# Optimization experiments

Measured on AMD Instinct MI355X. Metric: run time of the kernel, lower is better.

## Reference

```python
import jax, jax.numpy as jnp
import numpy as np
import math

B, S, D, H = 1, 2048, 2048, 16
HD = D // H  # head_dim = 128


def _rotate_half(x):
    h = x.shape[-1] // 2
    return jnp.concatenate([-x[..., h:], x[..., :h]], axis=-1)


def setup_inputs() -> dict:
    key = jax.random.key(0)
    ks = jax.random.split(key, 8)
    hidden_states = jax.random.normal(ks[0], (B, S, D), dtype=jnp.float32)
    # additive causal mask: 0 on/below diagonal, large negative above
    causal = jnp.tril(jnp.ones((S, S), dtype=bool))
    attention_mask = jnp.where(causal, 0.0, -1e9).astype(jnp.float32)[None, None]
    # LLaMA rotary tables for head_dim
    inv_freq = 1.0 / (10000.0 ** (jnp.arange(0, HD, 2, dtype=jnp.float32) / HD))
    t = jnp.arange(S, dtype=jnp.float32)
    freqs = jnp.einsum('s,d->sd', t, inv_freq)          # [S, HD/2]
    emb = jnp.concatenate([freqs, freqs], axis=-1)       # [S, HD]
    cos = jnp.cos(emb)[None, None]                       # [1,1,S,HD]
    sin = jnp.sin(emb)[None, None]
    scale = 1.0 / math.sqrt(D)
    Wq = jax.random.normal(ks[1], (D, D), dtype=jnp.float32) * scale
    Wk = jax.random.normal(ks[2], (D, D), dtype=jnp.float32) * scale
    Wv = jax.random.normal(ks[3], (D, D), dtype=jnp.float32) * scale
    Wo = jax.random.normal(ks[4], (D, D), dtype=jnp.float32) * scale
    # IA3 scales initialized to ones (as in module), perturbed slightly to be non-trivial
    l_k = jnp.ones((1, H, 1, HD), dtype=jnp.float32) + 0.01 * jax.random.normal(ks[5], (1, H, 1, HD), dtype=jnp.float32)
    l_v = jnp.ones((1, H, 1, HD), dtype=jnp.float32) + 0.01 * jax.random.normal(ks[6], (1, H, 1, HD), dtype=jnp.float32)
    return {
        'hidden_states': hidden_states, 'attention_mask': attention_mask,
        'cos': cos, 'sin': sin,
        'Wq': Wq, 'Wk': Wk, 'Wv': Wv, 'Wo': Wo, 'l_k': l_k, 'l_v': l_v,
    }


def reference(hidden_states, attention_mask, cos, sin, Wq, Wk, Wv, Wo, l_k, l_v):
    b, s, d = hidden_states.shape
    h, hd = H, HD
    # projections (nn.Linear: x @ W.T), split heads -> [b, h, s, hd]
    def split_heads(x):
        return x.reshape(b, s, h, hd).transpose(0, 2, 1, 3)
    q = split_heads(hidden_states @ Wq.T)
    k = split_heads(hidden_states @ Wk.T)
    v = split_heads(hidden_states @ Wv.T)
    # RoPE on q and k
    q = q * cos + _rotate_half(q) * sin
    k = k * cos + _rotate_half(k) * sin
    # IA3: note the module scales QUERY by peft_l_k and VALUE by peft_l_v
    q = q * l_k
    v = v * l_v
    # manual attention
    scores = jnp.einsum('bhqd,bhkd->bhqk', q, k) / math.sqrt(hd)
    scores = scores + attention_mask
    attn = jax.nn.softmax(scores.astype(jnp.float32), axis=-1).astype(scores.dtype)
    out = jnp.einsum('bhqk,bhkd->bhqd', attn, v)
    out = out.transpose(0, 2, 1, 3).reshape(b, s, d)
    return out @ Wo.T
```

## Files before the change

kernel.cpp:

```cpp
#include <hip/hip_runtime.h>

typedef __attribute__((ext_vector_type(8))) short short8;
typedef __attribute__((ext_vector_type(4))) short s16x4;
typedef __attribute__((ext_vector_type(4))) float f32x4;
typedef unsigned short ushort;

#define S_LEN 2048
#define D_MODEL 2048
#define NH 16
#define HD 128

__device__ __forceinline__ float b2f(ushort u) {
  union { unsigned int i; float f; } v; v.i = ((unsigned int)u) << 16; return v.f;
}
__device__ __forceinline__ ushort f2b(float f) {
  union { float f; unsigned int i; } v; v.f = f;
  unsigned int r = v.i + 0x7FFFu + ((v.i >> 16) & 1u);
  return (ushort)(r >> 16);
}
__device__ __forceinline__ ushort f2b_trunc(float f) {
  union { float f; unsigned int i; } v; v.f = f;
  return (ushort)(v.i >> 16);
}

__device__ __forceinline__ void gload_lds16(const void* g, void* l) {
  __builtin_amdgcn_global_load_lds(
      (const __attribute__((address_space(1))) void*)g,
      (__attribute__((address_space(3))) void*)l, 16, 0, 0);
}

template<bool C32, bool QKVM>
__device__ __forceinline__ void gemm_bf16_body(const ushort* __restrict__ A,
                                               const ushort* __restrict__ B,
                                               void* __restrict__ Cp, int ldc,
                                               const float* __restrict__ lv,
                                               const float* __restrict__ cosb,
                                               const float* __restrict__ sinb,
                                               const float* __restrict__ lk)
{
  __shared__ ushort lA[128 * 64];
  __shared__ ushort lB[128 * 64];
  const int tid  = threadIdx.x;
  const int lane = tid & 63;
  const int wave = tid >> 6;
  const int quad = lane >> 4;
  const int l15  = lane & 15;
  const int wm   = wave >> 1;
  const int wn   = wave & 1;
  const int m0   = blockIdx.y * 128;
  const int n0   = blockIdx.x * 128;

  const bool isV = QKVM && (n0 >= 4096);
  int bcol[4];
#pragma unroll
  for (int j = 0; j < 4; ++j)
    bcol[j] = (QKVM && !isV) ? (wn * 32 + (j & 1) * 16 + (j >> 1) * 64)
                             : (wn * 64 + j * 16);

  f32x4 acc[4][4];
#pragma unroll
  for (int i = 0; i < 4; ++i)
#pragma unroll
    for (int j = 0; j < 4; ++j)
      acc[i][j] = (f32x4){0.f, 0.f, 0.f, 0.f};

  const int srow0 = wave * 8 + (lane >> 3);
  const int cph   = lane & 7;

  for (int kt = 0; kt < 32; ++kt) {
    __syncthreads();
#pragma unroll
    for (int j = 0; j < 4; ++j) {
      const int row = j * 32 + srow0;
      const int gc  = cph ^ (row & 7);
      gload_lds16(A + (size_t)(m0 + row) * 2048 + kt * 64 + gc * 8,
                  &lA[row * 64 + cph * 8]);
      gload_lds16(B + (size_t)(n0 + row) * 2048 + kt * 64 + gc * 8,
                  &lB[row * 64 + cph * 8]);
    }
    __syncthreads();
#pragma unroll
    for (int kk = 0; kk < 2; ++kk) {
      short8 af[4], bfr[4];
#pragma unroll
      for (int i = 0; i < 4; ++i) {
        const int r = wm * 64 + i * 16 + l15;
        af[i] = *(const short8*)&lA[r * 64 + (((kk * 4 + quad) ^ (l15 & 7)) * 8)];
      }
#pragma unroll
      for (int j = 0; j < 4; ++j) {
        const int r = bcol[j] + l15;
        bfr[j] = *(const short8*)&lB[r * 64 + (((kk * 4 + quad) ^ (l15 & 7)) * 8)];
      }
#pragma unroll
      for (int i = 0; i < 4; ++i)
#pragma unroll
        for (int j = 0; j < 4; ++j)
          acc[i][j] = __builtin_amdgcn_mfma_f32_16x16x32_bf16(af[i], bfr[j], acc[i][j], 0, 0, 0);
    }
  }

  if (QKVM) {
    ushort* C = (ushort*)Cp;
    if (isV) {
#pragma unroll
      for (int j = 0; j < 4; ++j)
#pragma unroll
        for (int i = 0; i < 4; ++i) {
          const int vcol = n0 - 4096 + bcol[j] + l15;
          const float sc = lv[vcol];
          const int sb   = m0 + wm * 64 + i * 16 + quad * 4;
          s16x4 pk;
#pragma unroll
          for (int r = 0; r < 4; ++r) pk[r] = (short)f2b(acc[i][j][r] * sc);
          *(s16x4*)&C[(size_t)vcol * 6144 + 4096 + sb] = pk;
        }
    } else {
      const bool isQ = (n0 < 2048);
      const int hb = n0 & 2047;
      const float qsc = 0.08838834764831845f * 1.4426950408889634f;
#pragma unroll
      for (int i = 0; i < 4; ++i)
#pragma unroll
        for (int j = 0; j < 2; ++j) {
          const int d_lo = bcol[j] + l15;
          const int d_hi = d_lo + 64;
          const float sl_lo = isQ ? lk[hb + d_lo] * qsc : 1.f;
          const float sl_hi = isQ ? lk[hb + d_hi] * qsc : 1.f;
#pragma unroll
          for (int r = 0; r < 4; ++r) {
            const int s = m0 + wm * 64 + i * 16 + quad * 4 + r;
            const float c_lo = cosb[s * HD + d_lo], s_lo = sinb[s * HD + d_lo];
            const float c_hi = cosb[s * HD + d_hi], s_hi = sinb[s * HD + d_hi];
            const float lo = acc[i][j][r];
            const float hi = acc[i][j + 2][r];
            float o_lo = lo * c_lo - hi * s_lo;
            float o_hi = hi * c_hi + lo * s_hi;
            if (isQ) { o_lo *= sl_lo; o_hi *= sl_hi; }
            C[(size_t)s * 6144 + n0 + d_lo] = f2b(o_lo);
            C[(size_t)s * 6144 + n0 + d_hi] = f2b(o_hi);
          }
        }
    }
    return;
  }

#pragma unroll
  for (int i = 0; i < 4; ++i)
#pragma unroll
    for (int j = 0; j < 4; ++j)
#pragma unroll
      for (int r = 0; r < 4; ++r) {
        const int row = m0 + wm * 64 + i * 16 + quad * 4 + r;
        const int col = n0 + bcol[j] + l15;
        if (C32) ((float*)Cp)[(size_t)row * ldc + col] = acc[i][j][r];
        else     ((ushort*)Cp)[(size_t)row * ldc + col] = f2b(acc[i][j][r]);
      }
}

__global__ __launch_bounds__(256)
void gemm_qkv_b(const ushort* __restrict__ A, const ushort* __restrict__ B,
                ushort* __restrict__ C, const float* __restrict__ lv,
                const float* __restrict__ cosb, const float* __restrict__ sinb,
                const float* __restrict__ lk)
{ gemm_bf16_body<false, true>(A, B, C, 6144, lv, cosb, sinb, lk); }

__global__ __launch_bounds__(256)
void gemm_bf16_f(const ushort* __restrict__ A, const ushort* __restrict__ B,
                 float* __restrict__ C, int ldc)
{ gemm_bf16_body<true, false>(A, B, C, ldc, nullptr, nullptr, nullptr, nullptr); }

__global__ __launch_bounds__(256)
void cvt_to_bf16(const float* __restrict__ hs, const float* __restrict__ Wq,
                 const float* __restrict__ Wk, const float* __restrict__ Wv,
                 const float* __restrict__ Wo, ushort* __restrict__ dst)
{
  const size_t base = ((size_t)blockIdx.x * 256 + threadIdx.x) * 8;
  const int row = (int)(base >> 11);
  const int col = (int)(base & 2047);
  const float* src;
  if      (row < 2048) src = Wq + (size_t)row * 2048;
  else if (row < 4096) src = Wk + (size_t)(row - 2048) * 2048;
  else if (row < 6144) src = Wv + (size_t)(row - 4096) * 2048;
  else if (row < 8192) src = Wo + (size_t)(row - 6144) * 2048;
  else                 src = hs + (size_t)(row - 8192) * 2048;
  float4 a = *(const float4*)(src + col);
  float4 b = *(const float4*)(src + col + 4);
  short8 s;
  s[0] = (short)f2b(a.x); s[1] = (short)f2b(a.y);
  s[2] = (short)f2b(a.z); s[3] = (short)f2b(a.w);
  s[4] = (short)f2b(b.x); s[5] = (short)f2b(b.y);
  s[6] = (short)f2b(b.z); s[7] = (short)f2b(b.w);
  *(short8*)(dst + base) = s;
}

__device__ const int FA_QT[30]   = {5,11,11,10,10,15,15,4,9,9,13,14,14,14,15,8,8,12,12,13,13,3,7,7,12,6,6,2,1,0};
__device__ const int FA_BEG[30]  = {0,0,12,0,11,10,21,0,0,10,18,0,10,20,0,0,9,8,17,0,9,0,0,8,0,0,7,0,0,0};
__device__ const int FA_END[30]  = {12,12,24,11,22,21,32,10,10,20,28,10,20,30,10,9,18,17,26,9,18,8,8,16,8,7,14,6,4,2};
__device__ const int FA_SLOT[30] = {5,16,17,14,15,28,29,4,12,13,23,24,25,26,27,10,11,19,20,21,22,3,8,9,18,6,7,2,1,0};
__device__ const int FA_OFF[16]  = {0,1,2,3,4,5,6,8,10,12,14,16,18,21,24,27};
__device__ const int FA_NC[16]   = {1,1,1,1,1,1,2,2,2,2,2,2,3,3,3,3};

__global__ __launch_bounds__(256, 2)
void flash_attn2(const ushort* __restrict__ arena,
                 ushort* __restrict__ Ab,
                 ushort* __restrict__ Opart,
                 float* __restrict__ Ml)
{
  __shared__ ushort Kl[64 * 128];
  __shared__ ushort Vt[128 * 64];
  __shared__ ushort Pl[4][32 * 72];

  const int tid  = threadIdx.x;
  const int lane = tid & 63;
  const int w    = tid >> 6;
  const int quad = lane >> 4;
  const int l15  = lane & 15;
  const int h    = blockIdx.y;

  const int item  = blockIdx.x;
  const int qt    = FA_QT[item];
  const int ktBeg = FA_BEG[item];
  const int ktEnd = FA_END[item];
  const int slot  = h * 30 + FA_SLOT[item];

  short8 qa[2][4];
#pragma unroll
  for (int i = 0; i < 2; ++i)
#pragma unroll
    for (int kk = 0; kk < 4; ++kk)
      qa[i][kk] = *(const short8*)(arena +
          (size_t)(qt * 128 + w * 32 + i * 16 + l15) * 6144 + h * HD + kk * 32 + quad * 8);

  f32x4 o[2][8], acc_l[2];
#pragma unroll
  for (int i = 0; i < 2; ++i) {
    acc_l[i] = (f32x4){0.f, 0.f, 0.f, 0.f};
#pragma unroll
    for (int nf = 0; nf < 8; ++nf) o[i][nf] = (f32x4){0.f, 0.f, 0.f, 0.f};
  }

  short8 bones;
#pragma unroll
  for (int e = 0; e < 8; ++e) bones[e] = (short)0x3F80;

  const int ksrow0 = w * 4 + (lane >> 4);
  const int kch    = lane & 15;
  const int vrow0  = w * 8 + (lane >> 3);
  const int vch    = lane & 7;

  for (int kt = ktBeg; kt < ktEnd; ++kt) {
    __syncthreads();

#pragma unroll
    for (int j = 0; j < 4; ++j) {
      const int row = j * 16 + ksrow0;
      const int gc  = kch ^ (row & 15);
      gload_lds16(arena + (size_t)(kt * 64 + row) * 6144 + 2048 + h * HD + gc * 8,
                  &Kl[row * 128 + kch * 8]);
    }
#pragma unroll
    for (int j = 0; j < 4; ++j) {
      const int d  = j * 32 + vrow0;
      const int gc = vch ^ (d & 7);
      gload_lds16(arena + (size_t)(h * HD + d) * 6144 + 4096 + kt * 64 + gc * 8,
                  &Vt[d * 64 + vch * 8]);
    }
    __syncthreads();

    f32x4 sf[2][4];
#pragma unroll
    for (int i = 0; i < 2; ++i)
#pragma unroll
      for (int n = 0; n < 4; ++n) sf[i][n] = (f32x4){0.f, 0.f, 0.f, 0.f};
#pragma unroll
    for (int kk = 0; kk < 4; ++kk)
#pragma unroll
      for (int n = 0; n < 4; ++n) {
        const int key = n * 16 + l15;
        short8 b = *(const short8*)&Kl[key * 128 + (((kk * 4 + quad) ^ l15) * 8)];
#pragma unroll
        for (int i = 0; i < 2; ++i)
          sf[i][n] = __builtin_amdgcn_mfma_f32_16x16x32_bf16(qa[i][kk], b, sf[i][n], 0, 0, 0);
      }

    if (kt >= 2 * qt) {
#pragma unroll
      for (int i = 0; i < 2; ++i)
#pragma unroll
        for (int n = 0; n < 4; ++n)
#pragma unroll
          for (int r = 0; r < 4; ++r) {
            const int key = kt * 64 + n * 16 + l15;
            const int row = qt * 128 + w * 32 + i * 16 + quad * 4 + r;
            if (key > row) sf[i][n][r] = -1e30f;
          }
    }

#pragma unroll
    for (int i = 0; i < 2; ++i)
#pragma unroll
      for (int n = 0; n < 4; ++n)
#pragma unroll
        for (int r = 0; r < 4; ++r)
          Pl[w][(i * 16 + quad * 4 + r) * 72 + n * 16 + l15] = f2b_trunc(exp2f(sf[i][n][r]));

#pragma unroll
    for (int kk = 0; kk < 2; ++kk) {
      short8 pa[2];
#pragma unroll
      for (int i = 0; i < 2; ++i)
        pa[i] = *(const short8*)&Pl[w][(i * 16 + l15) * 72 + kk * 32 + quad * 8];
#pragma unroll
      for (int nf = 0; nf < 8; ++nf) {
        const int d = nf * 16 + l15;
        short8 b = *(const short8*)&Vt[d * 64 + (((kk * 4 + quad) ^ (l15 & 7)) * 8)];
#pragma unroll
        for (int i = 0; i < 2; ++i)
          o[i][nf] = __builtin_amdgcn_mfma_f32_16x16x32_bf16(pa[i], b, o[i][nf], 0, 0, 0);
      }
#pragma unroll
      for (int i = 0; i < 2; ++i)
        acc_l[i] = __builtin_amdgcn_mfma_f32_16x16x32_bf16(pa[i], bones, acc_l[i], 0, 0, 0);
    }
  }

  if (FA_NC[qt] == 1) {
    float inv[2][4];
#pragma unroll
    for (int i = 0; i < 2; ++i)
#pragma unroll
      for (int r = 0; r < 4; ++r) inv[i][r] = 1.0f / acc_l[i][r];
#pragma unroll
    for (int i = 0; i < 2; ++i)
#pragma unroll
      for (int nf = 0; nf < 8; ++nf)
#pragma unroll
        for (int r = 0; r < 4; ++r) {
          const int row = qt * 128 + w * 32 + i * 16 + quad * 4 + r;
          const int col = h * HD + nf * 16 + l15;
          Ab[(size_t)row * 2048 + col] = f2b(o[i][nf][r] * inv[i][r]);
        }
  } else {
    ushort* dst = Opart + (size_t)slot * (128 * 128);
#pragma unroll
    for (int i = 0; i < 2; ++i)
#pragma unroll
      for (int nf = 0; nf < 8; ++nf)
#pragma unroll
        for (int r = 0; r < 4; ++r) {
          const int row = w * 32 + i * 16 + quad * 4 + r;
          const int col = nf * 16 + l15;
          dst[row * 128 + col] = f2b(o[i][nf][r]);
        }
    if (l15 == 0) {
#pragma unroll
      for (int i = 0; i < 2; ++i)
#pragma unroll
        for (int r = 0; r < 4; ++r)
          Ml[(size_t)slot * 128 + w * 32 + i * 16 + quad * 4 + r] = acc_l[i][r];
    }
  }
}

__global__ __launch_bounds__(256)
void fa_combine2(const ushort* __restrict__ Opart, const float* __restrict__ Ml,
                 ushort* __restrict__ Ab)
{
  const int qt  = 6 + blockIdx.x;
  const int h   = blockIdx.y;
  const int row = threadIdx.x >> 1;
  const int hf  = (threadIdx.x & 1) * 64;
  const int np  = FA_NC[qt];
  const int s0  = h * 30 + FA_OFF[qt];

  float lsum = 0.f;
  for (int c = 0; c < np; ++c) lsum += Ml[(size_t)(s0 + c) * 128 + row];
  const float inv = 1.0f / lsum;

  float acc[64];
#pragma unroll
  for (int e = 0; e < 64; ++e) acc[e] = 0.f;
  for (int c = 0; c < np; ++c) {
    const ushort* src = Opart + (size_t)(s0 + c) * (128 * 128) + row * 128 + hf;
#pragma unroll
    for (int j = 0; j < 8; ++j) {
      short8 x = *(const short8*)(src + j * 8);
#pragma unroll
      for (int e = 0; e < 8; ++e) acc[j * 8 + e] += b2f((ushort)x[e]);
    }
  }
  ushort* d = Ab + (size_t)(qt * 128 + row) * 2048 + h * 128 + hf;
#pragma unroll
  for (int j = 0; j < 8; ++j) {
    short8 y;
#pragma unroll
    for (int e = 0; e < 8; ++e) y[e] = (short)f2b(acc[j * 8 + e] * inv);
    *(short8*)(d + j * 8) = y;
  }
}

template<bool A32, bool B32, bool C32>
__device__ __forceinline__ void gemm_body(const void* __restrict__ Ap,
                                          const void* __restrict__ Bp,
                                          void* __restrict__ Cp)
{
  __shared__ ushort lA[128 * 72];
  __shared__ ushort lB[128 * 72];
  const int tid  = threadIdx.x;
  const int lane = tid & 63;
  const int wave = tid >> 6;
  const int quad = lane >> 4;
  const int l15  = lane & 15;
  const int wm   = wave >> 1;
  const int wn   = wave & 1;
  const int m0   = blockIdx.y * 128;
  const int n0   = blockIdx.x * 128;

  f32x4 acc[4][4];
#pragma unroll
  for (int i = 0; i < 4; ++i)
#pragma unroll
    for (int j = 0; j < 4; ++j)
      acc[i][j] = (f32x4){0.f, 0.f, 0.f, 0.f};

  const int srow = tid >> 1;
  const int scol = (tid & 1) * 32;
  ushort* aL = &lA[srow * 72 + scol];
  ushort* bL = &lB[srow * 72 + scol];

  for (int kt = 0; kt < 32; ++kt) {
    __syncthreads();
    if (A32) {
      const float* g = (const float*)Ap + (size_t)(m0 + srow) * 2048 + kt * 64 + scol;
#pragma unroll
      for (int j = 0; j < 4; ++j) {
        float4 f0 = *(const float4*)(g + 8 * j);
        float4 f1 = *(const float4*)(g + 8 * j + 4);
        short8 sv;
        sv[0] = (short)f2b(f0.x); sv[1] = (short)f2b(f0.y);
        sv[2] = (short)f2b(f0.z); sv[3] = (short)f2b(f0.w);
        sv[4] = (short)f2b(f1.x); sv[5] = (short)f2b(f1.y);
        sv[6] = (short)f2b(f1.z); sv[7] = (short)f2b(f1.w);
        *(short8*)(aL + 8 * j) = sv;
      }
    } else {
      const ushort* g = (const ushort*)Ap + (size_t)(m0 + srow) * 2048 + kt * 64 + scol;
#pragma unroll
      for (int j = 0; j < 4; ++j)
        *(short8*)(aL + 8 * j) = *(const short8*)(g + 8 * j);
    }
    if (B32) {
      const float* g = (const float*)Bp + (size_t)(n0 + srow) * 2048 + kt * 64 + scol;
#pragma unroll
      for (int j = 0; j < 4; ++j) {
        float4 f0 = *(const float4*)(g + 8 * j);
        float4 f1 = *(const float4*)(g + 8 * j + 4);
        short8 sv;
        sv[0] = (short)f2b(f0.x); sv[1] = (short)f2b(f0.y);
        sv[2] = (short)f2b(f0.z); sv[3] = (short)f2b(f0.w);
        sv[4] = (short)f2b(f1.x); sv[5] = (short)f2b(f1.y);
        sv[6] = (short)f2b(f1.z); sv[7] = (short)f2b(f1.w);
        *(short8*)(bL + 8 * j) = sv;
      }
    } else {
      const ushort* g = (const ushort*)Bp + (size_t)(n0 + srow) * 2048 + kt * 64 + scol;
#pragma unroll
      for (int j = 0; j < 4; ++j)
        *(short8*)(bL + 8 * j) = *(const short8*)(g + 8 * j);
    }
    __syncthreads();
#pragma unroll
    for (int kk = 0; kk < 2; ++kk) {
      short8 af[4], bfr[4];
#pragma unroll
      for (int i = 0; i < 4; ++i)
        af[i] = *(const short8*)&lA[(wm * 64 + i * 16 + l15) * 72 + kk * 32 + quad * 8];
#pragma unroll
      for (int j = 0; j < 4; ++j)
        bfr[j] = *(const short8*)&lB[(wn * 64 + j * 16 + l15) * 72 + kk * 32 + quad * 8];
#pragma unroll
      for (int i = 0; i < 4; ++i)
#pragma unroll
        for (int j = 0; j < 4; ++j)
          acc[i][j] = __builtin_amdgcn_mfma_f32_16x16x32_bf16(af[i], bfr[j], acc[i][j], 0, 0, 0);
    }
  }

#pragma unroll
  for (int i = 0; i < 4; ++i)
#pragma unroll
    for (int j = 0; j < 4; ++j)
#pragma unroll
      for (int r = 0; r < 4; ++r) {
        const int row = m0 + wm * 64 + i * 16 + quad * 4 + r;
        const int col = n0 + wn * 64 + j * 16 + l15;
        if (C32) ((float*)Cp)[(size_t)row * 2048 + col] = acc[i][j][r];
        else     ((ushort*)Cp)[(size_t)row * 2048 + col] = f2b(acc[i][j][r]);
      }
}

__global__ __launch_bounds__(256)
void gemm_qkv_f32(const float* __restrict__ A, const float* __restrict__ Bq,
                  const float* __restrict__ Bk, const float* __restrict__ Bv,
                  ushort* __restrict__ Cq, ushort* __restrict__ Ck, ushort* __restrict__ Cv)
{
  const float* B = (blockIdx.z == 0) ? Bq : (blockIdx.z == 1 ? Bk : Bv);
  ushort* C      = (blockIdx.z == 0) ? Cq : (blockIdx.z == 1 ? Ck : Cv);
  gemm_body<true, true, false>(A, B, C);
}

__global__ __launch_bounds__(256)
void gemm_wo_f32(const ushort* __restrict__ A, const float* __restrict__ B,
                 float* __restrict__ C)
{ gemm_body<false, true, true>(A, B, C); }

__global__ __launch_bounds__(256)
void rope_ia3_old(ushort* __restrict__ base, int stride, int koff, int voff,
                  const float* __restrict__ cosb, const float* __restrict__ sinb,
                  const float* __restrict__ lk, const float* __restrict__ lv)
{
  const int s = blockIdx.x;
  const float qscale = 0.08838834764831845f * 1.4426950408889634f;
#pragma unroll
  for (int i = 0; i < 4; ++i) {
    const int p = threadIdx.x + 256 * i;
    const int h = p >> 6;
    const int d = p & 63;
    const size_t lo = (size_t)s * stride + h * HD + d;
    const size_t hi = lo + 64;
    const float c_lo = cosb[s * HD + d];
    const float c_hi = cosb[s * HD + d + 64];
    const float s_lo = sinb[s * HD + d];
    const float s_hi = sinb[s * HD + d + 64];
    ushort* Q = base;
    ushort* K = base + koff;
    ushort* V = base + voff;
    const float qlo = b2f(Q[lo]), qhi = b2f(Q[hi]);
    const float klo = b2f(K[lo]), khi = b2f(K[hi]);
    const float vlo = b2f(V[lo]), vhi = b2f(V[hi]);
    const float rq_lo = qlo * c_lo - qhi * s_lo;
    const float rq_hi = qhi * c_hi + qlo * s_hi;
    const float rk_lo = klo * c_lo - khi * s_lo;
    const float rk_hi = khi * c_hi + klo * s_hi;
    Q[lo] = f2b(rq_lo * lk[h * HD + d]      * qscale);
    Q[hi] = f2b(rq_hi * lk[h * HD + d + 64] * qscale);
    K[lo] = f2b(rk_lo);
    K[hi] = f2b(rk_hi);
    V[lo] = f2b(vlo * lv[h * HD + d]);
    V[hi] = f2b(vhi * lv[h * HD + d + 64]);
  }
}

__global__ __launch_bounds__(256)
void flash_attn_old(const ushort* __restrict__ QKV, int stride, int koff, int voff,
                    ushort* __restrict__ Ob, int ostride)
{
  __shared__ ushort Kl[64 * 128];
  __shared__ ushort Vt[128 * 64];
  __shared__ ushort Pl[4][16 * 72];

  const int tid  = threadIdx.x;
  const int lane = tid & 63;
  const int w    = tid >> 6;
  const int quad = lane >> 4;
  const int l15  = lane & 15;
  const int qt   = (int)gridDim.x - 1 - (int)blockIdx.x;
  const int h    = blockIdx.y;

  const ushort* Q = QKV;
  const ushort* K = QKV + koff;
  const ushort* V = QKV + voff;

  const int qrow = qt * 64 + w * 16 + l15;
  short8 qa[4];
#pragma unroll
  for (int kk = 0; kk < 4; ++kk)
    qa[kk] = *(const short8*)(Q + (size_t)qrow * stride + h * HD + kk * 32 + quad * 8);

  float m_[4], l_[4];
  f32x4 o[8];
#pragma unroll
  for (int r = 0; r < 4; ++r) { m_[r] = -1e30f; l_[r] = 0.f; }
#pragma unroll
  for (int nf = 0; nf < 8; ++nf) o[nf] = (f32x4){0.f, 0.f, 0.f, 0.f};

  const int ksrow0 = w * 4 + (lane >> 4);
  const int kch    = lane & 15;
  const int vkp    = tid & 15;
  const int vd8    = tid >> 4;

  for (int kt = 0; kt <= qt; ++kt) {
    __syncthreads();
#pragma unroll
    for (int j = 0; j < 4; ++j) {
      const int row = j * 16 + ksrow0;
      const int gc  = kch ^ (row & 15);
      gload_lds16(K + (size_t)(kt * 64 + row) * stride + h * HD + gc * 8,
                  &Kl[row * 128 + kch * 8]);
    }
    {
      const ushort* vb = V + (size_t)(kt * 64) * stride + h * HD + vd8 * 8;
      short8 v0 = *(const short8*)(vb + (size_t)(2 * vkp)      * stride);
      short8 v1 = *(const short8*)(vb + (size_t)(2 * vkp + 1)  * stride);
      short8 v2 = *(const short8*)(vb + (size_t)(2 * vkp + 32) * stride);
      short8 v3 = *(const short8*)(vb + (size_t)(2 * vkp + 33) * stride);
      const int wlo = vkp >> 2, woff = 2 * (vkp & 3);
#pragma unroll
      for (int c = 0; c < 8; ++c) {
        const int d = vd8 * 8 + c;
        unsigned int p01 = (ushort)v0[c] | ((unsigned int)(ushort)v1[c] << 16);
        unsigned int p23 = (ushort)v2[c] | ((unsigned int)(ushort)v3[c] << 16);
        *(unsigned int*)&Vt[d * 64 + ((wlo       ^ c) * 8) + woff] = p01;
        *(unsigned int*)&Vt[d * 64 + (((wlo + 4) ^ c) * 8) + woff] = p23;
      }
    }
    __syncthreads();

    f32x4 sf[4];
#pragma unroll
    for (int n = 0; n < 4; ++n) sf[n] = (f32x4){0.f, 0.f, 0.f, 0.f};
#pragma unroll
    for (int kk = 0; kk < 4; ++kk)
#pragma unroll
      for (int n = 0; n < 4; ++n) {
        const int key = n * 16 + l15;
        short8 b = *(const short8*)&Kl[key * 128 + (((kk * 4 + quad) ^ l15) * 8)];
        sf[n] = __builtin_amdgcn_mfma_f32_16x16x32_bf16(qa[kk], b, sf[n], 0, 0, 0);
      }

    if (kt == qt) {
#pragma unroll
      for (int n = 0; n < 4; ++n)
#pragma unroll
        for (int r = 0; r < 4; ++r)
          if (n * 16 + l15 > w * 16 + quad * 4 + r) sf[n][r] = -1e30f;
    }

    float pm[4];
#pragma unroll
    for (int r = 0; r < 4; ++r)
      pm[r] = fmaxf(fmaxf(sf[0][r], sf[1][r]), fmaxf(sf[2][r], sf[3][r]));
#pragma unroll
    for (int off = 1; off < 16; off <<= 1)
#pragma unroll
      for (int r = 0; r < 4; ++r)
        pm[r] = fmaxf(pm[r], __shfl_xor(pm[r], off));

    float al[4], ps[4], p[4][4];
#pragma unroll
    for (int r = 0; r < 4; ++r) {
      const float mn = fmaxf(m_[r], pm[r]);
      al[r] = exp2f(m_[r] - mn);
      m_[r] = mn;
      ps[r] = 0.f;
    }
#pragma unroll
    for (int n = 0; n < 4; ++n)
#pragma unroll
      for (int r = 0; r < 4; ++r) {
        p[n][r] = exp2f(sf[n][r] - m_[r]);
        ps[r] += p[n][r];
      }
#pragma unroll
    for (int off = 1; off < 16; off <<= 1)
#pragma unroll
      for (int r = 0; r < 4; ++r)
        ps[r] += __shfl_xor(ps[r], off);
#pragma unroll
    for (int r = 0; r < 4; ++r) l_[r] = al[r] * l_[r] + ps[r];
#pragma unroll
    for (int nf = 0; nf < 8; ++nf)
#pragma unroll
      for (int r = 0; r < 4; ++r) o[nf][r] *= al[r];

#pragma unroll
    for (int n = 0; n < 4; ++n)
#pragma unroll
      for (int r = 0; r < 4; ++r)
        Pl[w][(quad * 4 + r) * 72 + n * 16 + l15] = f2b(p[n][r]);

#pragma unroll
    for (int kk = 0; kk < 2; ++kk) {
      short8 pa = *(const short8*)&Pl[w][l15 * 72 + kk * 32 + quad * 8];
#pragma unroll
      for (int nf = 0; nf < 8; ++nf) {
        const int d = nf * 16 + l15;
        short8 b = *(const short8*)&Vt[d * 64 + (((kk * 4 + quad) ^ (l15 & 7)) * 8)];
        o[nf] = __builtin_amdgcn_mfma_f32_16x16x32_bf16(pa, b, o[nf], 0, 0, 0);
      }
    }
  }

  float inv[4];
#pragma unroll
  for (int r = 0; r < 4; ++r) inv[r] = 1.0f / l_[r];
#pragma unroll
  for (int nf = 0; nf < 8; ++nf)
#pragma unroll
    for (int r = 0; r < 4; ++r) {
      const int row = qt * 64 + w * 16 + quad * 4 + r;
      const int col = h * HD + nf * 16 + l15;
      Ob[(size_t)row * ostride + col] = f2b(o[nf][r] * inv[r]);
    }
}

extern "C" void kernel_launch(void* const* d_in, const int* in_sizes, int n_in,
                              void* d_out, int out_size, void* d_ws, size_t ws_size,
                              hipStream_t stream)
{
  const float* hs   = (const float*)d_in[0];
  const float* cosb = (const float*)d_in[2];
  const float* sinb = (const float*)d_in[3];
  const float* Wq   = (const float*)d_in[4];
  const float* Wk   = (const float*)d_in[5];
  const float* Wv   = (const float*)d_in[6];
  const float* Wo   = (const float*)d_in[7];
  const float* lk   = (const float*)d_in[8];
  const float* lv   = (const float*)d_in[9];
  float* out = (float*)d_out;

  char* ws = (char*)d_ws;
  const bool fast = ws_size >= (size_t)64 * 1024 * 1024;

  if (fast) {
    ushort* WB    = (ushort*)ws;
    ushort* hsB   = WB + (size_t)8192 * 2048;
    ushort* QKV   = (ushort*)(ws + (size_t)40 * 1024 * 1024);
    ushort* Ab    = hsB;
    ushort* Opart = WB;
    float*  Ml    = (float*)(ws + (size_t)16 * 1024 * 1024);

    cvt_to_bf16<<<dim3(10240), 256, 0, stream>>>(hs, Wq, Wk, Wv, Wo, WB);
    gemm_qkv_b<<<dim3(48, 16), 256, 0, stream>>>(hsB, WB, QKV, lv, cosb, sinb, lk);
    flash_attn2<<<dim3(30, NH), 256, 0, stream>>>(QKV, Ab, Opart, Ml);
    fa_combine2<<<dim3(10, NH), 256, 0, stream>>>(Opart, Ml, Ab);
    gemm_bf16_f<<<dim3(16, 16), 256, 0, stream>>>(Ab, WB + (size_t)6144 * 2048, out, 2048);
  } else {
    const size_t SZ = (size_t)S_LEN * D_MODEL;
    ushort* Qb = (ushort*)ws;
    ushort* Kb = Qb + SZ;
    ushort* Vb = Qb + 2 * SZ;
    ushort* Ab = Qb;

    gemm_qkv_f32<<<dim3(16, 16, 3), 256, 0, stream>>>(hs, Wq, Wk, Wv, Qb, Kb, Vb);
    rope_ia3_old<<<dim3(S_LEN), 256, 0, stream>>>(Qb, 2048, (int)SZ, (int)(2 * SZ), cosb, sinb, lk, lv);
    flash_attn_old<<<dim3(S_LEN / 64, NH), 256, 0, stream>>>(Qb, 2048, (int)SZ, (int)(2 * SZ), Ab, 2048);
    gemm_wo_f32<<<dim3(16, 16), 256, 0, stream>>>(Ab, Wo, out);
  }
}
```

Baseline: 307.5 us.

## Transpose RoPE tables for vector loads and use 128x64 tiles for output GEMM

The conversion kernel now also writes transposed cos/sin tables into the output buffer as scratch. The QKV GEMM epilogue can then read four consecutive sequence positions per lane with one vector load, replacing the earlier strided scalar loads. The output projection GEMM moves to a 128x64 tile with 512 blocks instead of 256, to fill more compute units at the cost of more total A-tile traffic. Using the output buffer as temporary storage is safe only because the final GEMM overwrites it.

```diff
diff --git a/kernel.cpp b/kernel.cpp
--- a/kernel.cpp
+++ b/kernel.cpp
@@ -29,14 +29,11 @@
       (__attribute__((address_space(3))) void*)l, 16, 0, 0);
 }
 
-template<bool C32, bool QKVM>
-__device__ __forceinline__ void gemm_bf16_body(const ushort* __restrict__ A,
-                                               const ushort* __restrict__ B,
-                                               void* __restrict__ Cp, int ldc,
-                                               const float* __restrict__ lv,
-                                               const float* __restrict__ cosb,
-                                               const float* __restrict__ sinb,
-                                               const float* __restrict__ lk)
+__global__ __launch_bounds__(256)
+void gemm_qkv_b(const ushort* __restrict__ A, const ushort* __restrict__ B,
+                ushort* __restrict__ C, const float* __restrict__ lv,
+                const float* __restrict__ cosT, const float* __restrict__ sinT,
+                const float* __restrict__ lk)
 {
   __shared__ ushort lA[128 * 64];
   __shared__ ushort lB[128 * 64];
@@ -50,12 +47,12 @@
   const int m0   = blockIdx.y * 128;
   const int n0   = blockIdx.x * 128;
 
-  const bool isV = QKVM && (n0 >= 4096);
+  const bool isV = (n0 >= 4096);
   int bcol[4];
 #pragma unroll
   for (int j = 0; j < 4; ++j)
-    bcol[j] = (QKVM && !isV) ? (wn * 32 + (j & 1) * 16 + (j >> 1) * 64)
-                             : (wn * 64 + j * 16);
+    bcol[j] = isV ? (wn * 64 + j * 16)
+                  : (wn * 32 + (j & 1) * 16 + (j >> 1) * 64);
 
   f32x4 acc[4][4];
 #pragma unroll
@@ -100,81 +97,148 @@
     }
   }
 
-  if (QKVM) {
-    ushort* C = (ushort*)Cp;
-    if (isV) {
-#pragma unroll
-      for (int j = 0; j < 4; ++j)
-#pragma unroll
-        for (int i = 0; i < 4; ++i) {
-          const int vcol = n0 - 4096 + bcol[j] + l15;
-          const float sc = lv[vcol];
-          const int sb   = m0 + wm * 64 + i * 16 + quad * 4;
-          s16x4 pk;
-#pragma unroll
-          for (int r = 0; r < 4; ++r) pk[r] = (short)f2b(acc[i][j][r] * sc);
-          *(s16x4*)&C[(size_t)vcol * 6144 + 4096 + sb] = pk;
-        }
-    } else {
-      const bool isQ = (n0 < 2048);
-      const int hb = n0 & 2047;
-      const float qsc = 0.08838834764831845f * 1.4426950408889634f;
+  if (isV) {
+#pragma unroll
+    for (int j = 0; j < 4; ++j)
+#pragma unroll
+      for (int i = 0; i < 4; ++i) {
+        const int vcol = n0 - 4096 + bcol[j] + l15;
+        const float sc = lv[vcol];
+        const int sb   = m0 + wm * 64 + i * 16 + quad * 4;
+        s16x4 pk;
+#pragma unroll
+        for (int r = 0; r < 4; ++r) pk[r] = (short)f2b(acc[i][j][r] * sc);
+        *(s16x4*)&C[(size_t)vcol * 6144 + 4096 + sb] = pk;
+      }
+    return;
+  }
+
+  const bool isQ = (n0 < 2048);
+  const int hb = n0 & 2047;
+  const float qsc = 0.08838834764831845f * 1.4426950408889634f;
+#pragma unroll
+  for (int j = 0; j < 2; ++j) {
+    const int d_lo = bcol[j] + l15;
+    const int d_hi = d_lo + 64;
+    const float sl_lo = isQ ? lk[hb + d_lo] * qsc : 1.f;
+    const float sl_hi = isQ ? lk[hb + d_hi] * qsc : 1.f;
+#pragma unroll
+    for (int i = 0; i < 4; ++i) {
+      const int sb = m0 + wm * 64 + i * 16 + quad * 4;
+      const f32x4 cl = *(const f32x4*)&cosT[d_lo * 2048 + sb];
+      const f32x4 sl = *(const f32x4*)&sinT[d_lo * 2048 + sb];
+      const f32x4 ch = *(const f32x4*)&cosT[d_hi * 2048 + sb];
+      const f32x4 sh = *(const f32x4*)&sinT[d_hi * 2048 + sb];
+#pragma unroll
+      for (int r = 0; r < 4; ++r) {
+        const float lo = acc[i][j][r];
+        const float hi = acc[i][j + 2][r];
+        float o_lo = lo * cl[r] - hi * sl[r];
+        float o_hi = hi * ch[r] + lo * sh[r];
+        if (isQ) { o_lo *= sl_lo; o_hi *= sl_hi; }
+        const int s = sb + r;
+        C[(size_t)s * 6144 + n0 + d_lo] = f2b(o_lo);
+        C[(size_t)s * 6144 + n0 + d_hi] = f2b(o_hi);
+      }
+    }
+  }
+}
+
+__global__ __launch_bounds__(256)
+void gemm_wo_64(const ushort* __restrict__ A, const ushort* __restrict__ B,
+                float* __restrict__ C)
+{
+  __shared__ ushort lA[128 * 64];
+  __shared__ ushort lB[64 * 64];
+  const int tid  = threadIdx.x;
+  const int lane = tid & 63;
+  const int wave = tid >> 6;
+  const int quad = lane >> 4;
+  const int l15  = lane & 15;
+  const int wm   = wave >> 1;
+  const int wn   = wave & 1;
+  const int m0   = blockIdx.y * 128;
+  const int n0   = blockIdx.x * 64;
+
+  f32x4 acc[4][2];
+#pragma unroll
+  for (int i = 0; i < 4; ++i)
+#pragma unroll
+    for (int j = 0; j < 2; ++j)
+      acc[i][j] = (f32x4){0.f, 0.f, 0.f, 0.f};
+
+  const int srow0 = wave * 8 + (lane >> 3);
+  const int cph   = lane & 7;
+
+  for (int kt = 0; kt < 32; ++kt) {
+    __syncthreads();
+#pragma unroll
+    for (int j = 0; j < 4; ++j) {
+      const int row = j * 32 + srow0;
+      const int gc  = cph ^ (row & 7);
+      gload_lds16(A + (size_t)(m0 + row) * 2048 + kt * 64 + gc * 8,
+                  &lA[row * 64 + cph * 8]);
+    }
+#pragma unroll
+    for (int j = 0; j < 2; ++j) {
+      const int row = j * 32 + srow0;
+      const int gc  = cph ^ (row & 7);
+      gload_lds16(B + (size_t)(n0 + row) * 2048 + kt * 64 + gc * 8,
+                  &lB[row * 64 + cph * 8]);
+    }
+    __syncthreads();
+#pragma unroll
+    for (int kk = 0; kk < 2; ++kk) {
+      short8 af[4], bfr[2];
+#pragma unroll
+      for (int i = 0; i < 4; ++i) {
+        const int r = wm * 64 + i * 16 + l15;
+        af[i] = *(const short8*)&lA[r * 64 + (((kk * 4 + quad) ^ (l15 & 7)) * 8)];
+      }
+#pragma unroll
+      for (int j = 0; j < 2; ++j) {
+        const int r = wn * 32 + j * 16 + l15;
+        bfr[j] = *(const short8*)&lB[r * 64 + (((kk * 4 + quad) ^ (l15 & 7)) * 8)];
+      }
 #pragma unroll
       for (int i = 0; i < 4; ++i)
 #pragma unroll
-        for (int j = 0; j < 2; ++j) {
-          const int d_lo = bcol[j] + l15;
-          const int d_hi = d_lo + 64;
-          const float sl_lo = isQ ? lk[hb + d_lo] * qsc : 1.f;
-          const float sl_hi = isQ ? lk[hb + d_hi] * qsc : 1.f;
-#pragma unroll
-          for (int r = 0; r < 4; ++r) {
-            const int s = m0 + wm * 64 + i * 16 + quad * 4 + r;
-            const float c_lo = cosb[s * HD + d_lo], s_lo = sinb[s * HD + d_lo];
-            const float c_hi = cosb[s * HD + d_hi], s_hi = sinb[s * HD + d_hi];
-            const float lo = acc[i][j][r];
-            const float hi = acc[i][j + 2][r];
-            float o_lo = lo * c_lo - hi * s_lo;
-            float o_hi = hi * c_hi + lo * s_hi;
-            if (isQ) { o_lo *= sl_lo; o_hi *= sl_hi; }
-            C[(size_t)s * 6144 + n0 + d_lo] = f2b(o_lo);
-            C[(size_t)s * 6144 + n0 + d_hi] = f2b(o_hi);
-          }
-        }
-    }
-    return;
+        for (int j = 0; j < 2; ++j)
+          acc[i][j] = __builtin_amdgcn_mfma_f32_16x16x32_bf16(af[i], bfr[j], acc[i][j], 0, 0, 0);
+    }
   }
 
 #pragma unroll
   for (int i = 0; i < 4; ++i)
 #pragma unroll
-    for (int j = 0; j < 4; ++j)
+    for (int j = 0; j < 2; ++j)
 #pragma unroll
       for (int r = 0; r < 4; ++r) {
         const int row = m0 + wm * 64 + i * 16 + quad * 4 + r;
-        const int col = n0 + bcol[j] + l15;
-        if (C32) ((float*)Cp)[(size_t)row * ldc + col] = acc[i][j][r];
-        else     ((ushort*)Cp)[(size_t)row * ldc + col] = f2b(acc[i][j][r]);
-      }
-}
-
-__global__ __launch_bounds__(256)
-void gemm_qkv_b(const ushort* __restrict__ A, const ushort* __restrict__ B,
-                ushort* __restrict__ C, const float* __restrict__ lv,
-                const float* __restrict__ cosb, const float* __restrict__ sinb,
-                const float* __restrict__ lk)
-{ gemm_bf16_body<false, true>(A, B, C, 6144, lv, cosb, sinb, lk); }
-
-__global__ __launch_bounds__(256)
-void gemm_bf16_f(const ushort* __restrict__ A, const ushort* __restrict__ B,
-                 float* __restrict__ C, int ldc)
-{ gemm_bf16_body<true, false>(A, B, C, ldc, nullptr, nullptr, nullptr, nullptr); }
+        const int col = n0 + wn * 32 + j * 16 + l15;
+        C[(size_t)row * 2048 + col] = acc[i][j][r];
+      }
+}
 
 __global__ __launch_bounds__(256)
 void cvt_to_bf16(const float* __restrict__ hs, const float* __restrict__ Wq,
                  const float* __restrict__ Wk, const float* __restrict__ Wv,
-                 const float* __restrict__ Wo, ushort* __restrict__ dst)
-{
+                 const float* __restrict__ Wo, ushort* __restrict__ dst,
+                 const float* __restrict__ cosb, const float* __restrict__ sinb,
+                 float* __restrict__ cosT, float* __restrict__ sinT)
+{
+  if (blockIdx.x >= 10240) {
+    const int b2 = blockIdx.x - 10240;
+    const int d  = b2 & 127;
+    const float* src = (b2 < 128) ? cosb : sinb;
+    float* dstT      = (b2 < 128) ? cosT : sinT;
+#pragma unroll
+    for (int kk = 0; kk < 8; ++kk) {
+      const int s = kk * 256 + threadIdx.x;
+      dstT[d * 2048 + s] = src[s * 128 + d];
+    }
+    return;
+  }
   const size_t base = ((size_t)blockIdx.x * 256 + threadIdx.x) * 8;
   const int row = (int)(base >> 11);
   const int col = (int)(base & 2047);
@@ -730,12 +794,15 @@
     ushort* Ab    = hsB;
     ushort* Opart = WB;
     float*  Ml    = (float*)(ws + (size_t)16 * 1024 * 1024);
-
-    cvt_to_bf16<<<dim3(10240), 256, 0, stream>>>(hs, Wq, Wk, Wv, Wo, WB);
-    gemm_qkv_b<<<dim3(48, 16), 256, 0, stream>>>(hsB, WB, QKV, lv, cosb, sinb, lk);
+    float*  cosT  = out;
+    float*  sinT  = out + (size_t)128 * 2048;
+
+    cvt_to_bf16<<<dim3(10496), 256, 0, stream>>>(hs, Wq, Wk, Wv, Wo, WB,
+                                                 cosb, sinb, cosT, sinT);
+    gemm_qkv_b<<<dim3(48, 16), 256, 0, stream>>>(hsB, WB, QKV, lv, cosT, sinT, lk);
     flash_attn2<<<dim3(30, NH), 256, 0, stream>>>(QKV, Ab, Opart, Ml);
     fa_combine2<<<dim3(10, NH), 256, 0, stream>>>(Opart, Ml, Ab);
-    gemm_bf16_f<<<dim3(16, 16), 256, 0, stream>>>(Ab, WB + (size_t)6144 * 2048, out, 2048);
+    gemm_wo_64<<<dim3(32, 16), 256, 0, stream>>>(Ab, WB + (size_t)6144 * 2048, out);
   } else {
     const size_t SZ = (size_t)S_LEN * D_MODEL;
     ushort* Qb = (ushort*)ws;
```

Measured after the change: 334.2 us. 1.09x slower.
